# Performance work log

Hardware: AMD Instinct MI355X
Metric: run time of the kernel (lower is better)

The kernel has to match this reference:

```python
import math
import jax, jax.numpy as jnp
import numpy as np

B, N, D, O = 8, 2048, 128, 128


def setup_inputs() -> dict:
    key = jax.random.key(0)
    ks = jax.random.split(key, 8)
    s = 1.0 / math.sqrt(D)
    x = jax.random.normal(ks[0], (B, N, D), dtype=jnp.float32)
    A = jax.random.bernoulli(ks[1], 0.02, (B, N, N)).astype(jnp.float32)
    W_qk = jax.random.normal(ks[2], (D, D), dtype=jnp.float32) * s
    b_qk = jnp.zeros((D,), dtype=jnp.float32)
    W_l = jax.random.normal(ks[3], (D, O), dtype=jnp.float32) * s
    b_l = jnp.zeros((O,), dtype=jnp.float32)
    W_r = jax.random.normal(ks[4], (D, O), dtype=jnp.float32) * s
    W_d = jax.random.normal(ks[5], (1, D), dtype=jnp.float32)
    b_d = jnp.zeros((D,), dtype=jnp.float32)
    return {"x": x, "A": A, "W_qk": W_qk, "b_qk": b_qk, "W_l": W_l,
            "b_l": b_l, "W_r": W_r, "W_d": W_d, "b_d": b_d}


def reference(x, A, W_qk, b_qk, W_l, b_l, W_r, W_d, b_d):
    d = x.shape[-1]
    # degree gate: sigmoid(Linear(deg)) scales features
    deg = jnp.sum(A, axis=-1, keepdims=True)              # (B,N,1)
    gate = jax.nn.sigmoid(deg @ W_d + b_d)                # (B,N,D)
    xg = x * gate                                         # (B,N,D)
    # sigmoid QK projection and dense NxN scores
    QK = jax.nn.sigmoid(xg @ W_qk + b_qk)                 # (B,N,D)
    scores = jnp.einsum('bnd,bmd->bnm', QK, QK) / jnp.sqrt(jnp.float32(d))
    scores = scores * A                                   # adjacency mask
    attn = scores / (jnp.sum(scores, axis=-1, keepdims=True) + 1e-6)
    agg = jnp.einsum('bnm,bmd->bnd', attn, xg)            # (B,N,D)
    out = agg @ W_l + b_l + xg @ W_r                      # (B,N,O)
    # F.normalize(p=2, dim=-1): x / max(||x||, eps)
    nrm = jnp.linalg.norm(out, axis=-1, keepdims=True)
    return out / jnp.maximum(nrm, 1e-12)
```

## Files before the change

kernel.cpp:

```cpp
#include <hip/hip_runtime.h>
#include <hip/hip_bf16.h>

#define B_ 8
#define N_ 2048
#define D_ 128
#define NROW (B_*N_)

typedef __bf16 bf16;
typedef __bf16 bf16x8 __attribute__((ext_vector_type(8)));
typedef float f32x4 __attribute__((ext_vector_type(4)));

__device__ __forceinline__ float sigmoidf_(float x) {
    return 1.0f / (1.0f + __expf(-x));
}

__device__ __forceinline__ void g2l16(const bf16* g, void* l) {
    __builtin_amdgcn_global_load_lds(
        (const __attribute__((address_space(1))) unsigned int*)g,
        (__attribute__((address_space(3))) unsigned int*)l, 16, 0, 0);
}

__global__ __launch_bounds__(256) void k_wtrans(const float* __restrict__ Wqk,
        const float* __restrict__ Wl, const float* __restrict__ Wr,
        bf16* __restrict__ wqkT, bf16* __restrict__ wlT, bf16* __restrict__ wrT) {
    int m = blockIdx.x >> 3;
    int chunk = blockIdx.x & 7;
    const float* W = (m == 0) ? Wqk : (m == 1 ? Wl : Wr);
    bf16* WT = (m == 0) ? wqkT : (m == 1 ? wlT : wrT);
#pragma unroll
    for (int e = 0; e < 8; ++e) {
        int idx = e * 256 + threadIdx.x;
        int ol = idx >> 7;
        int i  = idx & 127;
        int o = chunk * 16 + ol;
        WT[o * 128 + i] = (bf16)W[i * 128 + o];
    }
}

__global__ __launch_bounds__(256) void k_deg_mask(const float* __restrict__ A,
        unsigned int* __restrict__ mask, float* __restrict__ deg) {
    const int row = blockIdx.x;
    const float* a = A + (size_t)row * N_;
    const int t = threadIdx.x, w = t >> 6, lane = t & 63;
    __shared__ int partial[4];
    int cnt = 0;
    unsigned int* mrow = mask + (size_t)row * (N_ / 32);
#pragma unroll
    for (int i = 0; i < N_ / 1024; ++i) {
        float4 v = *(const float4*)(a + i * 1024 + t * 4);
        unsigned long long nib = (unsigned long long)((v.x != 0.f) | ((v.y != 0.f) << 1) |
                                                      ((v.z != 0.f) << 2) | ((v.w != 0.f) << 3));
        unsigned long long p = nib << ((t & 15) * 4);
        p |= __shfl_xor(p, 1);
        p |= __shfl_xor(p, 2);
        p |= __shfl_xor(p, 4);
        p |= __shfl_xor(p, 8);
        if ((t & 15) == 0) {
            int idx = i * 32 + (t >> 4) * 2;
            mrow[idx] = (unsigned int)p;
            mrow[idx + 1] = (unsigned int)(p >> 32);
            cnt += __popcll(p);
        }
    }
    cnt += __shfl_xor(cnt, 16);
    cnt += __shfl_xor(cnt, 32);
    if (lane == 0) partial[w] = cnt;
    __syncthreads();
    if (t == 0) deg[row] = (float)(partial[0] + partial[1] + partial[2] + partial[3]);
}

__global__ __launch_bounds__(256) void k_proj(const float* __restrict__ x,
        const float* __restrict__ deg, const float* __restrict__ Wd,
        const float* __restrict__ bd, const bf16* __restrict__ wqkT,
        const float* __restrict__ bqk,
        bf16* __restrict__ qkG, bf16* __restrict__ xgG, bf16* __restrict__ xgTG) {
    __shared__ bf16 wq[128][136];
    __shared__ bf16 xgl[64][136];
    const int t = threadIdx.x, lane = t & 63, w = t >> 6;
    const int rowbase = blockIdx.x * 64;
    {
        int r = t >> 1, h = t & 1;
        const bf16* src = wqkT + r * 128 + h * 64;
#pragma unroll
        for (int k = 0; k < 64; k += 8)
            *(bf16x8*)&wq[r][h * 64 + k] = *(const bf16x8*)(src + k);
    }
#pragma unroll
    for (int e = 0; e < 32; ++e) {
        int idx = e * 256 + t;
        int rl = idx >> 7;
        int d  = idx & 127;
        size_t fr = (size_t)rowbase + rl;
        float g = sigmoidf_(deg[fr] * Wd[d] + bd[d]);
        float v = x[fr * 128 + d] * g;
        bf16 bv = (bf16)v;
        xgl[rl][d] = bv;
        xgG[fr * 128 + d] = bv;
    }
    __syncthreads();
    const int cIdx = lane & 15, g4 = lane >> 4;
    bf16x8 ax[4];
#pragma unroll
    for (int c = 0; c < 4; ++c)
        ax[c] = *(const bf16x8*)&xgl[w * 16 + cIdx][c * 32 + g4 * 8];
#pragma unroll
    for (int dsub = 0; dsub < 8; ++dsub) {
        f32x4 acc = {0.f, 0.f, 0.f, 0.f};
#pragma unroll
        for (int c = 0; c < 4; ++c) {
            bf16x8 bw = *(const bf16x8*)&wq[dsub * 16 + cIdx][c * 32 + g4 * 8];
            acc = __builtin_amdgcn_mfma_f32_16x16x32_bf16(ax[c], bw, acc, 0, 0, 0);
        }
        int col = dsub * 16 + cIdx;
        float bb = bqk[col];
#pragma unroll
        for (int r = 0; r < 4; ++r) {
            size_t row = (size_t)rowbase + w * 16 + g4 * 4 + r;
            qkG[row * 128 + col] = (bf16)sigmoidf_(acc[r] + bb);
        }
    }
    {
        int b = rowbase / N_;
        int nbase = rowbase % N_;
#pragma unroll
        for (int e = 0; e < 32; ++e) {
            int idx = e * 256 + t;
            int d  = idx >> 6;
            int nl = idx & 63;
            xgTG[((size_t)b * 128 + d) * N_ + nbase + nl] = xgl[nl][d];
        }
    }
}

__global__ __launch_bounds__(512, 2) void k_attn(const bf16* __restrict__ qkG,
        const bf16* __restrict__ xgTG, const unsigned int* __restrict__ mask32,
        bf16* __restrict__ aggG) {
    __shared__ __align__(16) char LDSC[148480];
    const int t = threadIdx.x, lane = t & 63, w = t >> 6;
    const int q = w >> 1, s = w & 1;
    const int cIdx = lane & 15, g4 = lane >> 4;
    const int bid = (blockIdx.x & 7) * 32 + (blockIdx.x >> 3);
    const int b = bid >> 5;
    const int rowbase = (bid & 31) * 64;
    const int R0 = rowbase + s * 32;

    const int sq = w & 3;
    const bool stq = (w < 4);

    auto do_stage = [&](int ts, int bbuf) {
        const int jbase = sq * 512 + ts * 32;
        if (stq) {
            const int rowi = lane >> 4;
            const int g = lane & 15;
#pragma unroll
            for (int i = 0; i < 8; ++i) {
                int row = i * 4 + rowi;
                const bf16* gsrc = qkG + ((size_t)(b * N_ + jbase + row)) * 128 + ((g ^ (row & 7)) << 3);
                g2l16(gsrc, LDSC + (bbuf * 4 + sq) * 8192 + i * 1024);
            }
        } else {
            const int di = lane >> 2;
            const int g = lane & 3;
#pragma unroll
            for (int i = 0; i < 8; ++i) {
                int d = i * 16 + di;
                const bf16* gsrc = xgTG + ((size_t)(b * 128 + d)) * N_ + jbase + ((g ^ ((d >> 2) & 3)) << 3);
                g2l16(gsrc, LDSC + 65536 + (bbuf * 4 + sq) * 8192 + i * 1024);
            }
        }
    };

    bf16x8 aq[2][4];
#pragma unroll
    for (int isub = 0; isub < 2; ++isub) {
        const bf16* src = qkG + ((size_t)(b * N_ + R0 + isub * 16 + cIdx)) * 128 + g4 * 8;
#pragma unroll
        for (int kc = 0; kc < 4; ++kc) aq[isub][kc] = *(const bf16x8*)(src + kc * 32);
    }
    const unsigned int* mrow = mask32 + ((size_t)(b * N_ + R0 + (lane & 31))) * (N_ / 32) + q * 16;
    unsigned int mw_cur = (lane < 32) ? mrow[0] : 0u;

    do_stage(0, 0);
    __syncthreads();

    f32x4 num[2][8];
#pragma unroll
    for (int i = 0; i < 2; ++i)
#pragma unroll
        for (int jd = 0; jd < 8; ++jd) num[i][jd] = {0.f, 0.f, 0.f, 0.f};
    float rs[2][4] = {{0.f, 0.f, 0.f, 0.f}, {0.f, 0.f, 0.f, 0.f}};
    const float inv = 0.08838834764831845f;

    for (int ts = 0; ts < 16; ++ts) {
        const int bb = ts & 1;
        unsigned int mw_nxt = 0;
        if (ts < 15) {
            mw_nxt = (lane < 32) ? mrow[ts + 1] : 0u;
            do_stage(ts + 1, bb ^ 1);
        }
        const char* qb = LDSC + (bb * 4 + q) * 8192;
        f32x4 sv[2][2];
#pragma unroll
        for (int i = 0; i < 2; ++i) { sv[i][0] = {0.f,0.f,0.f,0.f}; sv[i][1] = {0.f,0.f,0.f,0.f}; }
#pragma unroll
        for (int kc = 0; kc < 4; ++kc) {
#pragma unroll
            for (int csub = 0; csub < 2; ++csub) {
                int jl = csub * 16 + cIdx;
                bf16x8 bq = *(const bf16x8*)(qb + jl * 256 + ((((kc << 2) | g4) ^ (jl & 7)) << 4));
                sv[0][csub] = __builtin_amdgcn_mfma_f32_16x16x32_bf16(aq[0][kc], bq, sv[0][csub], 0, 0, 0);
                sv[1][csub] = __builtin_amdgcn_mfma_f32_16x16x32_bf16(aq[1][kc], bq, sv[1][csub], 0, 0, 0);
            }
        }
        char* pb = LDSC + 131072 + w * 2048;
#pragma unroll
        for (int isub = 0; isub < 2; ++isub)
#pragma unroll
        for (int r = 0; r < 4; ++r) {
            int rl = isub * 16 + g4 * 4 + r;
            unsigned int mwv = __shfl(mw_cur, rl);
#pragma unroll
            for (int csub = 0; csub < 2; ++csub) {
                float v = sv[isub][csub][r] * inv;
                v = ((mwv >> (csub * 16 + cIdx)) & 1u) ? v : 0.0f;
                rs[isub][r] += v;
                *(bf16*)(pb + rl * 64 + ((((csub << 1) | (cIdx >> 3)) ^ ((rl >> 2) & 3)) << 4)
                         + ((cIdx & 7) << 1)) = (bf16)v;
            }
        }
        const char* xb = LDSC + 65536 + (bb * 4 + q) * 8192;
        bf16x8 ap[2];
#pragma unroll
        for (int isub = 0; isub < 2; ++isub) {
            int rl = isub * 16 + cIdx;
            ap[isub] = *(const bf16x8*)(pb + rl * 64 + ((g4 ^ ((rl >> 2) & 3)) << 4));
        }
#pragma unroll
        for (int dsub = 0; dsub < 8; ++dsub) {
            int d = dsub * 16 + cIdx;
            bf16x8 bx = *(const bf16x8*)(xb + d * 64 + ((g4 ^ ((d >> 2) & 3)) << 4));
            num[0][dsub] = __builtin_amdgcn_mfma_f32_16x16x32_bf16(ap[0], bx, num[0][dsub], 0, 0, 0);
            num[1][dsub] = __builtin_amdgcn_mfma_f32_16x16x32_bf16(ap[1], bx, num[1][dsub], 0, 0, 0);
        }
        mw_cur = mw_nxt;
        __syncthreads();
    }

#pragma unroll
    for (int isub = 0; isub < 2; ++isub)
#pragma unroll
    for (int r = 0; r < 4; ++r) {
        float v = rs[isub][r];
        v += __shfl_xor(v, 1); v += __shfl_xor(v, 2); v += __shfl_xor(v, 4); v += __shfl_xor(v, 8);
        rs[isub][r] = v;
    }
    float* RSB = (float*)(LDSC + 147456);
    if (cIdx == 0) {
#pragma unroll
        for (int isub = 0; isub < 2; ++isub)
#pragma unroll
        for (int r = 0; r < 4; ++r)
            RSB[(s * 32 + isub * 16 + g4 * 4 + r) * 4 + q] = rs[isub][r];
    }
    float* PART = (float*)LDSC;
#pragma unroll
    for (int isub = 0; isub < 2; ++isub)
#pragma unroll
    for (int dsub = 0; dsub < 8; ++dsub)
#pragma unroll
    for (int r = 0; r < 4; ++r)
        PART[q * 8192 + (s * 32 + isub * 16 + g4 * 4 + r) * 128 + dsub * 16 + cIdx] = num[isub][dsub][r];
    __syncthreads();
    {
        int row = t >> 3, colbase = (t & 7) * 16;
        float accv[16];
#pragma unroll
        for (int k = 0; k < 16; ++k) accv[k] = 0.f;
#pragma unroll
        for (int q4 = 0; q4 < 4; ++q4)
#pragma unroll
            for (int k = 0; k < 4; ++k) {
                f32x4 pv = *(const f32x4*)(PART + q4 * 8192 + row * 128 + colbase + k * 4);
                accv[k * 4 + 0] += pv[0]; accv[k * 4 + 1] += pv[1];
                accv[k * 4 + 2] += pv[2]; accv[k * 4 + 3] += pv[3];
            }
        float den = RSB[row * 4 + 0] + RSB[row * 4 + 1] + RSB[row * 4 + 2] + RSB[row * 4 + 3] + 1e-6f;
        float sc = 1.0f / den;
        bf16x8 o0, o1;
#pragma unroll
        for (int k = 0; k < 8; ++k) { o0[k] = (bf16)(accv[k] * sc); o1[k] = (bf16)(accv[8 + k] * sc); }
        bf16* dst = aggG + ((size_t)(b * N_ + rowbase + row)) * 128 + colbase;
        *(bf16x8*)dst = o0;
        *(bf16x8*)(dst + 8) = o1;
    }
}

__global__ __launch_bounds__(256) void k_out(const bf16* __restrict__ aggG,
        const bf16* __restrict__ xgG, const bf16* __restrict__ wlT,
        const bf16* __restrict__ wrT, const float* __restrict__ blv,
        float* __restrict__ out) {
    __shared__ bf16 wl[128][136];
    __shared__ bf16 wr[128][136];
    __shared__ bf16 ag[64][136];
    __shared__ bf16 xgl[64][136];
    const int t = threadIdx.x, lane = t & 63, w = t >> 6;
    const int rowbase = blockIdx.x * 64;
    {
        int r = t >> 1, h = t & 1;
#pragma unroll
        for (int k = 0; k < 64; k += 8) {
            *(bf16x8*)&wl[r][h * 64 + k] = *(const bf16x8*)(wlT + r * 128 + h * 64 + k);
            *(bf16x8*)&wr[r][h * 64 + k] = *(const bf16x8*)(wrT + r * 128 + h * 64 + k);
        }
        int rl = t >> 2, q = t & 3;
        const bf16* s1 = aggG + ((size_t)(rowbase + rl)) * 128 + q * 32;
        const bf16* s2 = xgG + ((size_t)(rowbase + rl)) * 128 + q * 32;
#pragma unroll
        for (int k = 0; k < 32; k += 8) {
            *(bf16x8*)&ag[rl][q * 32 + k] = *(const bf16x8*)(s1 + k);
            *(bf16x8*)&xgl[rl][q * 32 + k] = *(const bf16x8*)(s2 + k);
        }
    }
    __syncthreads();
    const int cIdx = lane & 15, g4 = lane >> 4;
    bf16x8 aa[4], ax[4];
#pragma unroll
    for (int c = 0; c < 4; ++c) {
        aa[c] = *(const bf16x8*)&ag[w * 16 + cIdx][c * 32 + g4 * 8];
        ax[c] = *(const bf16x8*)&xgl[w * 16 + cIdx][c * 32 + g4 * 8];
    }
    f32x4 acc[8];
    float ss[4] = {0.f, 0.f, 0.f, 0.f};
#pragma unroll
    for (int osub = 0; osub < 8; ++osub) {
        float bb = blv[osub * 16 + cIdx];
        f32x4 a = {bb, bb, bb, bb};
#pragma unroll
        for (int c = 0; c < 4; ++c) {
            bf16x8 b1 = *(const bf16x8*)&wl[osub * 16 + cIdx][c * 32 + g4 * 8];
            a = __builtin_amdgcn_mfma_f32_16x16x32_bf16(aa[c], b1, a, 0, 0, 0);
            bf16x8 b2 = *(const bf16x8*)&wr[osub * 16 + cIdx][c * 32 + g4 * 8];
            a = __builtin_amdgcn_mfma_f32_16x16x32_bf16(ax[c], b2, a, 0, 0, 0);
        }
        acc[osub] = a;
#pragma unroll
        for (int r = 0; r < 4; ++r) ss[r] += a[r] * a[r];
    }
#pragma unroll
    for (int r = 0; r < 4; ++r) {
        ss[r] += __shfl_xor(ss[r], 1);
        ss[r] += __shfl_xor(ss[r], 2);
        ss[r] += __shfl_xor(ss[r], 4);
        ss[r] += __shfl_xor(ss[r], 8);
    }
    float sc[4];
#pragma unroll
    for (int r = 0; r < 4; ++r) sc[r] = 1.0f / fmaxf(sqrtf(ss[r]), 1e-12f);
#pragma unroll
    for (int osub = 0; osub < 8; ++osub)
#pragma unroll
        for (int r = 0; r < 4; ++r) {
            size_t row = (size_t)rowbase + w * 16 + g4 * 4 + r;
            out[row * 128 + osub * 16 + cIdx] = acc[osub][r] * sc[r];
        }
}

extern "C" void kernel_launch(void* const* d_in, const int* in_sizes, int n_in,
                              void* d_out, int out_size, void* d_ws, size_t ws_size,
                              hipStream_t stream) {
    const float* x   = (const float*)d_in[0];
    const float* A   = (const float*)d_in[1];
    const float* Wqk = (const float*)d_in[2];
    const float* bqk = (const float*)d_in[3];
    const float* Wl  = (const float*)d_in[4];
    const float* bl  = (const float*)d_in[5];
    const float* Wr  = (const float*)d_in[6];
    const float* Wd  = (const float*)d_in[7];
    const float* bd  = (const float*)d_in[8];
    float* out = (float*)d_out;
    char* ws = (char*)d_ws;

    unsigned int* maskG = (unsigned int*)ws;
    float* degG = (float*)(ws + (4 << 20));
    bf16* wqkT  = (bf16*)(ws + (5 << 20));
    bf16* wlT   = (bf16*)(ws + (5 << 20) + 32768);
    bf16* wrT   = (bf16*)(ws + (5 << 20) + 65536);
    bf16* qkG   = (bf16*)(ws + (6 << 20));
    bf16* xgG   = (bf16*)(ws + (10 << 20));
    bf16* xgTG  = (bf16*)(ws + (14 << 20));
    bf16* aggG  = (bf16*)(ws + (18 << 20));

    hipLaunchKernelGGL(k_wtrans, dim3(24), dim3(256), 0, stream, Wqk, Wl, Wr, wqkT, wlT, wrT);
    hipLaunchKernelGGL(k_deg_mask, dim3(NROW), dim3(256), 0, stream, A, maskG, degG);
    hipLaunchKernelGGL(k_proj, dim3(NROW / 64), dim3(256), 0, stream,
                       x, degG, Wd, bd, wqkT, bqk, qkG, xgG, xgTG);
    hipLaunchKernelGGL(k_attn, dim3(NROW / 64), dim3(512), 0, stream, qkG, xgTG, maskG, aggG);
    hipLaunchKernelGGL(k_out, dim3(NROW / 64), dim3(256), 0, stream, aggG, xgG, wlT, wrT, bl, out);
}
```

Baseline: 262.2 us.

## Restructure attention kernel around 32x32x16 MFMA with register-resident probabilities

```diff
diff --git a/kernel.cpp b/kernel.cpp
--- a/kernel.cpp
+++ b/kernel.cpp
@@ -9,6 +9,7 @@
 typedef __bf16 bf16;
 typedef __bf16 bf16x8 __attribute__((ext_vector_type(8)));
 typedef float f32x4 __attribute__((ext_vector_type(4)));
+typedef float f32x16 __attribute__((ext_vector_type(16)));
 
 __device__ __forceinline__ float sigmoidf_(float x) {
     return 1.0f / (1.0f + __expf(-x));
@@ -18,6 +19,12 @@
     __builtin_amdgcn_global_load_lds(
         (const __attribute__((address_space(1))) unsigned int*)g,
         (__attribute__((address_space(3))) unsigned int*)l, 16, 0, 0);
+}
+
+__device__ __forceinline__ unsigned pk_bf16(float a, float b) {
+    union { bf16 h[2]; unsigned u; } t;
+    t.h[0] = (bf16)a; t.h[1] = (bf16)b;
+    return t.u;
 }
 
 __global__ __launch_bounds__(256) void k_wtrans(const float* __restrict__ Wqk,
@@ -135,141 +142,102 @@
 __global__ __launch_bounds__(512, 2) void k_attn(const bf16* __restrict__ qkG,
         const bf16* __restrict__ xgTG, const unsigned int* __restrict__ mask32,
         bf16* __restrict__ aggG) {
-    __shared__ __align__(16) char LDSC[148480];
-    const int t = threadIdx.x, lane = t & 63, w = t >> 6;
+    __shared__ __align__(16) char LDSC[132096];
+    const int t = threadIdx.x, l = t & 63, w = t >> 6;
+    const int h = l >> 5, l31 = l & 31;
     const int q = w >> 1, s = w & 1;
-    const int cIdx = lane & 15, g4 = lane >> 4;
     const int bid = (blockIdx.x & 7) * 32 + (blockIdx.x >> 3);
     const int b = bid >> 5;
     const int rowbase = (bid & 31) * 64;
     const int R0 = rowbase + s * 32;
-
-    const int sq = w & 3;
-    const bool stq = (w < 4);
-
-    auto do_stage = [&](int ts, int bbuf) {
-        const int jbase = sq * 512 + ts * 32;
-        if (stq) {
-            const int rowi = lane >> 4;
-            const int g = lane & 15;
-#pragma unroll
-            for (int i = 0; i < 8; ++i) {
-                int row = i * 4 + rowi;
-                const bf16* gsrc = qkG + ((size_t)(b * N_ + jbase + row)) * 128 + ((g ^ (row & 7)) << 3);
-                g2l16(gsrc, LDSC + (bbuf * 4 + sq) * 8192 + i * 1024);
-            }
-        } else {
-            const int di = lane >> 2;
-            const int g = lane & 3;
-#pragma unroll
-            for (int i = 0; i < 8; ++i) {
-                int d = i * 16 + di;
-                const bf16* gsrc = xgTG + ((size_t)(b * 128 + d)) * N_ + jbase + ((g ^ ((d >> 2) & 3)) << 3);
-                g2l16(gsrc, LDSC + 65536 + (bbuf * 4 + sq) * 8192 + i * 1024);
-            }
+    const float inv = 0.08838834764831845f;
+
+    auto do_stage = [&](int jb, int bbuf) {
+        char* qdst = LDSC + bbuf * 32768 + w * 4096;
+        char* xdst = LDSC + 65536 + bbuf * 32768 + w * 4096;
+#pragma unroll
+        for (int i = 0; i < 4; ++i) {
+            int G = w * 256 + i * 64 + l;
+            int j = G >> 4, g = G & 15;
+            const bf16* src = qkG + ((size_t)(b * N_ + jb + j)) * 128 + ((g ^ (j & 7)) << 3);
+            g2l16(src, qdst + i * 1024);
+            const bf16* src2 = xgTG + ((size_t)b * 128 + j) * N_ + jb + ((g ^ (j & 7)) << 3);
+            g2l16(src2, xdst + i * 1024);
         }
     };
 
-    bf16x8 aq[2][4];
-#pragma unroll
-    for (int isub = 0; isub < 2; ++isub) {
-        const bf16* src = qkG + ((size_t)(b * N_ + R0 + isub * 16 + cIdx)) * 128 + g4 * 8;
-#pragma unroll
-        for (int kc = 0; kc < 4; ++kc) aq[isub][kc] = *(const bf16x8*)(src + kc * 32);
-    }
-    const unsigned int* mrow = mask32 + ((size_t)(b * N_ + R0 + (lane & 31))) * (N_ / 32) + q * 16;
-    unsigned int mw_cur = (lane < 32) ? mrow[0] : 0u;
+    bf16x8 qki[8];
+    {
+        const bf16* srcB = qkG + ((size_t)(b * N_ + R0 + l31)) * 128 + h * 8;
+#pragma unroll
+        for (int sl = 0; sl < 8; ++sl) qki[sl] = *(const bf16x8*)(srcB + sl * 16);
+    }
+    const unsigned int* mrow = mask32 + ((size_t)(b * N_ + R0 + l31)) * (N_ / 32) + q;
+    unsigned int mw = mrow[0];
 
     do_stage(0, 0);
     __syncthreads();
 
-    f32x4 num[2][8];
-#pragma unroll
-    for (int i = 0; i < 2; ++i)
-#pragma unroll
-        for (int jd = 0; jd < 8; ++jd) num[i][jd] = {0.f, 0.f, 0.f, 0.f};
-    float rs[2][4] = {{0.f, 0.f, 0.f, 0.f}, {0.f, 0.f, 0.f, 0.f}};
-    const float inv = 0.08838834764831845f;
+    f32x16 num[4]; num[0] = f32x16{}; num[1] = f32x16{}; num[2] = f32x16{}; num[3] = f32x16{};
+    float rs = 0.f;
 
     for (int ts = 0; ts < 16; ++ts) {
         const int bb = ts & 1;
-        unsigned int mw_nxt = 0;
+        unsigned int mw_n = 0;
         if (ts < 15) {
-            mw_nxt = (lane < 32) ? mrow[ts + 1] : 0u;
-            do_stage(ts + 1, bb ^ 1);
-        }
-        const char* qb = LDSC + (bb * 4 + q) * 8192;
-        f32x4 sv[2][2];
-#pragma unroll
-        for (int i = 0; i < 2; ++i) { sv[i][0] = {0.f,0.f,0.f,0.f}; sv[i][1] = {0.f,0.f,0.f,0.f}; }
-#pragma unroll
-        for (int kc = 0; kc < 4; ++kc) {
-#pragma unroll
-            for (int csub = 0; csub < 2; ++csub) {
-                int jl = csub * 16 + cIdx;
-                bf16x8 bq = *(const bf16x8*)(qb + jl * 256 + ((((kc << 2) | g4) ^ (jl & 7)) << 4));
-                sv[0][csub] = __builtin_amdgcn_mfma_f32_16x16x32_bf16(aq[0][kc], bq, sv[0][csub], 0, 0, 0);
-                sv[1][csub] = __builtin_amdgcn_mfma_f32_16x16x32_bf16(aq[1][kc], bq, sv[1][csub], 0, 0, 0);
-            }
-        }
-        char* pb = LDSC + 131072 + w * 2048;
-#pragma unroll
-        for (int isub = 0; isub < 2; ++isub)
-#pragma unroll
-        for (int r = 0; r < 4; ++r) {
-            int rl = isub * 16 + g4 * 4 + r;
-            unsigned int mwv = __shfl(mw_cur, rl);
-#pragma unroll
-            for (int csub = 0; csub < 2; ++csub) {
-                float v = sv[isub][csub][r] * inv;
-                v = ((mwv >> (csub * 16 + cIdx)) & 1u) ? v : 0.0f;
-                rs[isub][r] += v;
-                *(bf16*)(pb + rl * 64 + ((((csub << 1) | (cIdx >> 3)) ^ ((rl >> 2) & 3)) << 4)
-                         + ((cIdx & 7) << 1)) = (bf16)v;
-            }
-        }
-        const char* xb = LDSC + 65536 + (bb * 4 + q) * 8192;
-        bf16x8 ap[2];
-#pragma unroll
-        for (int isub = 0; isub < 2; ++isub) {
-            int rl = isub * 16 + cIdx;
-            ap[isub] = *(const bf16x8*)(pb + rl * 64 + ((g4 ^ ((rl >> 2) & 3)) << 4));
-        }
-#pragma unroll
-        for (int dsub = 0; dsub < 8; ++dsub) {
-            int d = dsub * 16 + cIdx;
-            bf16x8 bx = *(const bf16x8*)(xb + d * 64 + ((g4 ^ ((d >> 2) & 3)) << 4));
-            num[0][dsub] = __builtin_amdgcn_mfma_f32_16x16x32_bf16(ap[0], bx, num[0][dsub], 0, 0, 0);
-            num[1][dsub] = __builtin_amdgcn_mfma_f32_16x16x32_bf16(ap[1], bx, num[1][dsub], 0, 0, 0);
-        }
-        mw_cur = mw_nxt;
+            mw_n = mrow[(ts + 1) * 4];
+            do_stage((ts + 1) * 128, bb ^ 1);
+        }
+        const char* qb = LDSC + bb * 32768;
+        const char* xb = LDSC + 65536 + bb * 32768;
+        f32x16 st{};
+        const int rowb = (q * 32 + l31) * 256;
+#pragma unroll
+        for (int sl = 0; sl < 8; ++sl) {
+            bf16x8 aj = *(const bf16x8*)(qb + rowb + ((((sl << 1) | h) ^ (l & 7)) << 4));
+            st = __builtin_amdgcn_mfma_f32_32x32x16_bf16(aj, qki[sl], st, 0, 0, 0);
+        }
+        unsigned int mws = mw >> (h * 4);
+        unsigned int wpk[8];
+#pragma unroll
+        for (int r2 = 0; r2 < 8; ++r2) {
+            const int r = r2 * 2;
+            const int bit0 = (r & 3) + 8 * (r >> 2);
+            float p0 = ((mws >> bit0) & 1u) ? st[r] * inv : 0.f;
+            float p1 = ((mws >> (bit0 + 1)) & 1u) ? st[r + 1] * inv : 0.f;
+            rs += p0 + p1;
+            wpk[r2] = pk_bf16(p0, p1);
+        }
+        union { unsigned int u[4]; bf16x8 v; } pa0, pa1;
+        pa0.u[0] = wpk[0]; pa0.u[1] = wpk[1]; pa0.u[2] = wpk[2]; pa0.u[3] = wpk[3];
+        pa1.u[0] = wpk[4]; pa1.u[1] = wpk[5]; pa1.u[2] = wpk[6]; pa1.u[3] = wpk[7];
+        const int xr = l & 7;
+#pragma unroll
+        for (int c = 0; c < 4; ++c) {
+            const char* rowp = xb + (c * 32 + l31) * 256;
+            union { unsigned long long d2[2]; bf16x8 v; } b0, b1;
+            b0.d2[0] = *(const unsigned long long*)(rowp + (((q * 4 + 0) ^ xr) << 4) + (h << 3));
+            b0.d2[1] = *(const unsigned long long*)(rowp + (((q * 4 + 1) ^ xr) << 4) + (h << 3));
+            b1.d2[0] = *(const unsigned long long*)(rowp + (((q * 4 + 2) ^ xr) << 4) + (h << 3));
+            b1.d2[1] = *(const unsigned long long*)(rowp + (((q * 4 + 3) ^ xr) << 4) + (h << 3));
+            num[c] = __builtin_amdgcn_mfma_f32_32x32x16_bf16(pa0.v, b0.v, num[c], 0, 0, 0);
+            num[c] = __builtin_amdgcn_mfma_f32_32x32x16_bf16(pa1.v, b1.v, num[c], 0, 0, 0);
+        }
+        mw = mw_n;
         __syncthreads();
     }
 
-#pragma unroll
-    for (int isub = 0; isub < 2; ++isub)
-#pragma unroll
-    for (int r = 0; r < 4; ++r) {
-        float v = rs[isub][r];
-        v += __shfl_xor(v, 1); v += __shfl_xor(v, 2); v += __shfl_xor(v, 4); v += __shfl_xor(v, 8);
-        rs[isub][r] = v;
-    }
-    float* RSB = (float*)(LDSC + 147456);
-    if (cIdx == 0) {
-#pragma unroll
-        for (int isub = 0; isub < 2; ++isub)
-#pragma unroll
-        for (int r = 0; r < 4; ++r)
-            RSB[(s * 32 + isub * 16 + g4 * 4 + r) * 4 + q] = rs[isub][r];
-    }
+    rs += __shfl_xor(rs, 32);
+    float* RSB = (float*)(LDSC + 131072);
+    if (l < 32) RSB[(s * 32 + l31) * 4 + q] = rs;
     float* PART = (float*)LDSC;
 #pragma unroll
-    for (int isub = 0; isub < 2; ++isub)
-#pragma unroll
-    for (int dsub = 0; dsub < 8; ++dsub)
-#pragma unroll
-    for (int r = 0; r < 4; ++r)
-        PART[q * 8192 + (s * 32 + isub * 16 + g4 * 4 + r) * 128 + dsub * 16 + cIdx] = num[isub][dsub][r];
+    for (int c = 0; c < 4; ++c)
+#pragma unroll
+        for (int r = 0; r < 16; ++r) {
+            int m = (r & 3) + 8 * (r >> 2) + 4 * h;
+            PART[q * 8192 + (s * 32 + m) * 128 + c * 32 + l31] = num[c][r];
+        }
     __syncthreads();
     {
         int row = t >> 3, colbase = (t & 7) * 16;
```

After: 255.2 us. 1.03x faster.
